# Performance work log

Hardware: AMD Instinct MI355X
Metric: run time of the kernel (lower is better)

The kernel has to match this reference:

```python
import jax, jax.numpy as jnp
import numpy as np

H = 5          # N_LSTM_nodes
NK = 32        # N_kernels
ND = 128       # N_dense_nodes
GH, GW = 20, 22


def _lstm_dir(x, Wih, Whh, b, reverse):
    # x: (P, in_dim); PyTorch gate order i, f, g, o; unbatched sequence of length P
    pre = x @ Wih.T + b  # (P, 4H) input contribution precomputed
    def step(carry, pt):
        h, c = carry
        g = pt + h @ Whh.T
        i, f, gg, o = jnp.split(g, 4)
        c = jax.nn.sigmoid(f) * c + jax.nn.sigmoid(i) * jnp.tanh(gg)
        h = jax.nn.sigmoid(o) * jnp.tanh(c)
        return (h, c), h
    z = jnp.zeros((H,), x.dtype)
    _, hs = jax.lax.scan(step, (z, z), pre, reverse=reverse)
    return hs  # (P, H), aligned with input order


def _bilstm(x, Wih, Whh, b):
    return jnp.concatenate([_lstm_dir(x, Wih[0], Whh[0], b[0], False),
                            _lstm_dir(x, Wih[1], Whh[1], b[1], True)], axis=-1)


def _conv(x, w, b, pad):
    y = jax.lax.conv_general_dilated(x, w, (1, 1), pad,
                                     dimension_numbers=('NCHW', 'OIHW', 'NCHW'))
    return y + b[None, :, None, None]


def _dense(x, w, b):
    return x @ w.T + b


def reference(Traces, Pstart, l0_Wih, l0_Whh, l0_b, l12_Wih, l12_Whh, l12_b,
              cw0, cb0, cw1, cb1, cw2, cb2, cw3, cb3,
              D1_w, D1_b, D2_w, D2_b, D3_w, D3_b,
              X1_w, X1_b, X2_w, X2_b, X3_w, X3_b,
              E1_w, E1_b, E2_w, E2_b, E3_w, E3_b,
              Xs, Ys, EventIndices, NEvents):
    lrelu, relu = jax.nn.leaky_relu, jax.nn.relu
    # 3-layer bidirectional LSTM over the concatenated pixel sequence
    x = _bilstm(Traces, l0_Wih, l0_Whh, l0_b)
    for l in range(2):
        x = _bilstm(x, l12_Wih[l], l12_Whh[l], l12_b[l])
    feat = x[:, 0]                                  # (P,)  LSTM_out[:, 0]
    P = feat.shape[0]
    # scatter: channels 0..H-1 get the LSTM feature, channel H gets Pstart
    vals = jnp.concatenate([jnp.broadcast_to(feat[:, None], (P, H)),
                            Pstart[:, None]], axis=1)          # (P, H+1)
    ch = jnp.arange(H + 1)
    Main = jnp.zeros((NEvents, H + 1, GH, GW), Traces.dtype)
    Main = Main.at[EventIndices[:, None], ch[None, :],
                   Xs[:, None], Ys[:, None]].set(vals)
    Main = jnp.where(jnp.isnan(Main), jnp.asarray(-1.0, Main.dtype), Main)
    Main = lrelu(_conv(Main, cw0, cb0, [(1, 1), (0, 0)]))  # (N, NK, 20, 20)
    Main = lrelu(_conv(Main, cw1, cb1, [(1, 1), (1, 1)]))
    Main = lrelu(_conv(Main, cw2, cb2, [(1, 1), (1, 1)]))
    Main = lrelu(_conv(Main, cw3, cb3, [(1, 1), (1, 1)]))
    Main = Main.reshape(NEvents, -1)                        # (N, NK*20*20)
    Main = relu(_dense(Main, D1_w, D1_b))
    Main = relu(_dense(Main, D2_w, D2_b))
    Main = relu(_dense(Main, D3_w, D3_b))
    Xm = relu(_dense(Main, X1_w, X1_b))
    Xm = relu(_dense(Xm, X2_w, X2_b))
    Xm = _dense(Xm, X3_w, X3_b)
    En = relu(_dense(Main, E1_w, E1_b))
    En = relu(_dense(En, E2_w, E2_b))
    En = _dense(En, E3_w, E3_b)
    out_w = jnp.ones((2,), Main.dtype)  # OutWeights = [1, 1]
    return jnp.concatenate([Xm, En], axis=1) * out_w


def setup_inputs() -> dict:
    key = jax.random.key(0)
    ks = jax.random.split(key, 40)
    P, N = 65536, 4096
    g = lambda i, shape, sc=0.1: jax.random.normal(ks[i], shape, jnp.float32) * sc
    return dict(
        Traces=jax.random.normal(ks[0], (P, 40), jnp.float32),
        Pstart=jax.random.uniform(ks[1], (P,), jnp.float32),
        l0_Wih=g(2, (2, 4 * H, 40)), l0_Whh=g(3, (2, 4 * H, H)), l0_b=g(4, (2, 4 * H)),
        l12_Wih=g(5, (2, 2, 4 * H, 2 * H)), l12_Whh=g(6, (2, 2, 4 * H, H)), l12_b=g(7, (2, 2, 4 * H)),
        cw0=g(8, (NK, H + 1, 3, 3)), cb0=g(9, (NK,)),
        cw1=g(10, (NK, NK, 3, 3)), cb1=g(11, (NK,)),
        cw2=g(12, (NK, NK, 3, 3)), cb2=g(13, (NK,)),
        cw3=g(14, (NK, NK, 3, 3)), cb3=g(15, (NK,)),
        D1_w=g(16, (ND, NK * 20 * 20), 0.01), D1_b=g(17, (ND,)),
        D2_w=g(18, (ND, ND)), D2_b=g(19, (ND,)),
        D3_w=g(20, (ND, ND)), D3_b=g(21, (ND,)),
        X1_w=g(22, (ND, ND)), X1_b=g(23, (ND,)),
        X2_w=g(24, (ND // 2, ND)), X2_b=g(25, (ND // 2,)),
        X3_w=g(26, (1, ND // 2)), X3_b=g(27, (1,)),
        E1_w=g(28, (ND, ND)), E1_b=g(29, (ND,)),
        E2_w=g(30, (ND // 2, ND)), E2_b=g(31, (ND // 2,)),
        E3_w=g(32, (1, ND // 2)), E3_b=g(33, (1,)),
        Xs=jax.random.randint(ks[34], (P,), 0, GH, jnp.int32),
        Ys=jax.random.randint(ks[35], (P,), 0, GW, jnp.int32),
        EventIndices=jnp.sort(jax.random.randint(ks[36], (P,), 0, N, jnp.int32)),
        NEvents=N,
    )
```

## Files before the change

kernel.cpp:

```cpp
#include <hip/hip_runtime.h>
#include <hip/hip_fp16.h>
#include <cstdint>
#include <cstddef>

#define PN 65536
#define NEV 4096
#define LCHUNK 4
#define LHALO 40
#define NCHUNK (PN / LCHUNK)
#define PRS 24

typedef _Float16 half8 __attribute__((ext_vector_type(8)));
typedef _Float16 half4 __attribute__((ext_vector_type(4)));
typedef float    f32x4 __attribute__((ext_vector_type(4)));
typedef float    f32x16 __attribute__((ext_vector_type(16)));

__device__ __forceinline__ float rcpf(float x)  { return __builtin_amdgcn_rcpf(x); }
__device__ __forceinline__ float sigf(float x)  { return rcpf(1.0f + __expf(-x)); }
__device__ __forceinline__ float tanh_(float x) { return 1.0f - 2.0f * rcpf(1.0f + __expf(2.0f * x)); }
__device__ __forceinline__ float lrelu(float x) { return x > 0.0f ? x : 0.01f * x; }

__global__ void k_preL(const float* __restrict__ hin, const float* __restrict__ wih,
                       const float* __restrict__ bb, _Float16* __restrict__ pre, int total) {
  int tid = blockIdx.x * 256 + threadIdx.x;
  if (tid >= total) return;
  int j = tid % 20;
  int p = (tid / 20) % PN;
  int d = tid / (20 * PN);
  const float2* h2 = (const float2*)(hin + (size_t)p * 10);
  const float2* w2 = (const float2*)(wih + (size_t)(d * 20 + j) * 10);
  float acc = bb[d * 20 + j];
  #pragma unroll
  for (int k = 0; k < 5; ++k) {
    float2 a = h2[k], b = w2[k];
    acc = fmaf(a.x, b.x, fmaf(a.y, b.y, acc));
  }
  pre[((size_t)d * PN + p) * PRS + j] = (_Float16)acc;
}

__global__ __launch_bounds__(64, 1) void k_scan(
    const _Float16* __restrict__ pre, const float* __restrict__ whh,
    float* __restrict__ hout, int hstride, int ncomp, int ndir) {
  int tid = blockIdx.x * 64 + threadIdx.x;
  if (tid >= ndir * NCHUNK) return;
  int d = tid / NCHUNK, c = tid % NCHUNK;
  float W[20][5];
  {
    const float4* wd4 = (const float4*)(whh + d * 100);
    float4 wv[25];
    #pragma unroll
    for (int i = 0; i < 25; ++i) wv[i] = wd4[i];
    float* wf = (float*)wv;
    #pragma unroll
    for (int j = 0; j < 20; ++j)
      #pragma unroll
      for (int k = 0; k < 5; ++k) W[j][k] = wf[j * 5 + k];
  }
  const _Float16* pd = pre + (size_t)d * PN * PRS;
  float h[5] = {0, 0, 0, 0, 0}, cs[5] = {0, 0, 0, 0, 0};
  int base = c * LCHUNK;
  int p, step, nsteps;
  if (d == 0) {
    int ps = base - LHALO; if (ps < 0) ps = 0;
    p = ps; step = 1; nsteps = base + LCHUNK - ps;
  } else {
    int ps = base + LCHUNK - 1 + LHALO; if (ps > PN - 1) ps = PN - 1;
    p = ps; step = -1; nsteps = ps - base + 1;
  }

  auto ld = [&](int pp, half8& A, half8& B, half4& C) {
    int pl = pp; if (pl < 0) pl = 0; if (pl >= PN) pl = PN - 1;
    const _Float16* rp = pd + (size_t)pl * PRS;
    A = *(const half8*)rp; B = *(const half8*)(rp + 8); C = *(const half4*)(rp + 16);
  };

  auto STEP = [&](half8 ca, half8 cb, half4 cc) {
    float g[20];
    #pragma unroll
    for (int i = 0; i < 8; ++i) { g[i] = (float)ca[i]; g[8 + i] = (float)cb[i]; }
    #pragma unroll
    for (int i = 0; i < 4; ++i) g[16 + i] = (float)cc[i];
    #pragma unroll
    for (int j = 0; j < 20; ++j) {
      #pragma unroll
      for (int k = 0; k < 5; ++k) g[j] = fmaf(W[j][k], h[k], g[j]);
    }
    #pragma unroll
    for (int k = 0; k < 5; ++k) {
      float it = sigf(g[k]);
      float ft = sigf(g[5 + k]);
      float gt = tanh_(g[10 + k]);
      float ot = sigf(g[15 + k]);
      cs[k] = fmaf(ft, cs[k], it * gt);
      h[k]  = ot * tanh_(cs[k]);
    }
    if ((unsigned)(p - base) < (unsigned)LCHUNK) {
      if (ncomp == 1) {
        hout[p] = h[0];
      } else {
        float* hp = hout + (size_t)p * hstride + d * 5;
        #pragma unroll
        for (int k = 0; k < 5; ++k) hp[k] = h[k];
      }
    }
    p += step;
  };

  half8 a0, a1, a2, a3, b0, b1, b2, b3;
  half4 c0, c1, c2, c3;
  ld(p,            a0, b0, c0);
  ld(p + step,     a1, b1, c1);
  ld(p + 2 * step, a2, b2, c2);
  ld(p + 3 * step, a3, b3, c3);

  for (int s = 0; s < nsteps; s += 4) {
    half8 na0, na1, na2, na3, nb0, nb1, nb2, nb3;
    half4 nc0, nc1, nc2, nc3;
    ld(p + 4 * step, na0, nb0, nc0);
    ld(p + 5 * step, na1, nb1, nc1);
    ld(p + 6 * step, na2, nb2, nc2);
    ld(p + 7 * step, na3, nb3, nc3);
    STEP(a0, b0, c0);
    STEP(a1, b1, c1);
    STEP(a2, b2, c2);
    STEP(a3, b3, c3);
    a0 = na0; b0 = nb0; c0 = nc0;
    a1 = na1; b1 = nb1; c1 = nc1;
    a2 = na2; b2 = nb2; c2 = nc2;
    a3 = na3; b3 = nb3; c3 = nc3;
  }
}

__global__ void k_scat2(const int* __restrict__ ei, const int* __restrict__ xs,
                        const int* __restrict__ ys, const int* __restrict__ owner,
                        const float* __restrict__ feat, const float* __restrict__ pstart,
                        _Float16* __restrict__ main0g) {
  int p = blockIdx.x * 256 + threadIdx.x;
  if (p >= PN) return;
  int e = ei[p];
  int cell = e * 440 + xs[p] * 22 + ys[p];
  if (owner[cell] != p) return;
  _Float16 f = (_Float16)feat[p];
  _Float16* b = main0g + (size_t)cell * 8;
  #pragma unroll
  for (int ch = 0; ch < 5; ++ch) b[ch] = f;
  b[5] = (_Float16)pstart[p];
}

#define PREP_F ((2 * PN * 20) / 256)
#define PREP_A ((NEV * 440 * 4) / 256)
#define PREP_G (PN / 256)
#define PREP_C 144
#define PREP_D (128 * 13)
#define PREP_E 320
__global__ __launch_bounds__(256) void k_prep(
    const float* __restrict__ tr, const float* __restrict__ l0_Wih,
    const float* __restrict__ l0_b, _Float16* __restrict__ pre,
    _Float16* __restrict__ main0g, int* __restrict__ owner,
    const int* __restrict__ ei, const int* __restrict__ xs, const int* __restrict__ ys,
    const float* __restrict__ cw0, const float* __restrict__ cw1,
    const float* __restrict__ cw2, const float* __restrict__ cw3,
    _Float16* __restrict__ wt,
    const float* __restrict__ D1w, _Float16* __restrict__ d1wt,
    const float* __restrict__ D2, const float* __restrict__ D3,
    const float* __restrict__ X1, const float* __restrict__ X2,
    const float* __restrict__ E1, const float* __restrict__ E2,
    _Float16* __restrict__ mlpw) {
  __shared__ float t[32][33];
  int b = blockIdx.x;
  if (b < PREP_F) {
    int tid = b * 256 + threadIdx.x;
    int j = tid % 20;
    int p = (tid / 20) % PN;
    int d = tid / (20 * PN);
    const float4* t4 = (const float4*)(tr + (size_t)p * 40);
    const float4* w4 = (const float4*)(l0_Wih + (size_t)(d * 20 + j) * 40);
    float acc = l0_b[d * 20 + j];
    #pragma unroll
    for (int k = 0; k < 10; ++k) {
      float4 a = t4[k], w = w4[k];
      acc = fmaf(a.x, w.x, fmaf(a.y, w.y, fmaf(a.z, w.z, fmaf(a.w, w.w, acc))));
    }
    pre[((size_t)d * PN + p) * PRS + j] = (_Float16)acc;
  } else if (b < PREP_F + PREP_A) {
    int i = (b - PREP_F) * 256 + threadIdx.x;
    ((uint32_t*)main0g)[i] = 0u;
  } else if (b < PREP_F + PREP_A + PREP_G) {
    int p = (b - PREP_F - PREP_A) * 256 + threadIdx.x;
    int cell = ei[p] * 440 + xs[p] * 22 + ys[p];
    atomicMax(&owner[cell], p);
  } else if (b < PREP_F + PREP_A + PREP_G + PREP_C) {
    int tid = (b - PREP_F - PREP_A - PREP_G) * 256 + threadIdx.x;
    if (tid < 4 * 9216) {
      int L = tid / 9216, r = tid % 9216;
      int ic = r & 31, oc = (r >> 5) & 31, kykx = r >> 10;
      const float* w = (L == 0) ? cw0 : (L == 1) ? cw1 : (L == 2) ? cw2 : cw3;
      int Cin = (L == 0) ? 6 : 32;
      float v = (ic < Cin) ? w[(oc * Cin + ic) * 9 + kykx] : 0.0f;
      wt[tid] = (_Float16)v;
    }
  } else if (b < PREP_F + PREP_A + PREP_G + PREP_C + PREP_D) {
    int j = b - PREP_F - PREP_A - PREP_G - PREP_C;
    int od = j / 13;
    int p0 = (j % 13) * 32;
    int tx = threadIdx.x & 31, ty = threadIdx.x >> 5;
    for (int oc = ty; oc < 32; oc += 8) {
      int pix = p0 + tx;
      t[oc][tx] = (pix < 400) ? D1w[(size_t)od * 12800 + oc * 400 + pix] : 0.0f;
    }
    __syncthreads();
    for (int pp = ty; pp < 32; pp += 8) {
      int pix = p0 + pp;
      if (pix < 400) d1wt[(size_t)od * 12800 + pix * 32 + tx] = (_Float16)t[tx][pp];
    }
  } else {
    int i = (b - PREP_F - PREP_A - PREP_G - PREP_C - PREP_D) * 256 + threadIdx.x;
    if (i < 81920) {
      const float* s; int off;
      if      (i < 16384) { s = D2; off = 0; }
      else if (i < 32768) { s = D3; off = 16384; }
      else if (i < 49152) { s = X1; off = 32768; }
      else if (i < 57344) { s = X2; off = 49152; }
      else if (i < 73728) { s = E1; off = 57344; }
      else                { s = E2; off = 73728; }
      mlpw[i] = (_Float16)s[i - off];
    }
  }
}

#define ARS 28
#define ACT_N (22 * ARS * 40)
__global__ __launch_bounds__(256, 2) void k_conv(
    const _Float16* __restrict__ main0g, const _Float16* __restrict__ wtall,
    const float* __restrict__ cb0, const float* __restrict__ cb1,
    const float* __restrict__ cb2, const float* __restrict__ cb3,
    _Float16* __restrict__ gbuf) {
  __shared__ _Float16 lds[ACT_N];
  int e   = blockIdx.x;
  int tid = threadIdx.x;
  int lane = tid & 63, wv = tid >> 6;
  int ln = lane & 31, s = lane >> 5;

  const uint4* src = (const uint4*)(main0g + (size_t)e * 440 * 8);
  uint4 sv0, sv1;
  int si0 = tid, si1 = tid + 256;
  if (si0 < 440) sv0 = src[si0];
  if (si1 < 440) sv1 = src[si1];

  for (int i = tid; i < 176; i += 256) {
    int row = (i >= 88) ? 21 : 0;
    int j = (i >= 88) ? i - 88 : i;
    int col = j >> 2, hb = (j & 3) * 8;
    *(uint4*)&lds[(row * ARS + col) * 40 + hb] = (uint4){0, 0, 0, 0};
  }
  for (int i = tid; i < 1320; i += 256) {
    int row = 1 + i / 66;
    int j = i % 66;
    int col = j / 3, hb = 8 + (j % 3) * 8;
    *(uint4*)&lds[(row * ARS + col) * 40 + hb] = (uint4){0, 0, 0, 0};
  }
  if (si0 < 440) {
    int r = si0 / 22, c = si0 - r * 22;
    *(uint4*)&lds[((r + 1) * ARS + c) * 40] = sv0;
  }
  if (si1 < 440) {
    int r = si1 / 22, c = si1 - r * 22;
    *(uint4*)&lds[((r + 1) * ARS + c) * 40] = sv1;
  }
  int pix[4]; bool val[4];
  #pragma unroll
  for (int t = 0; t < 4; ++t) {
    int tile = (t < 3) ? (wv + t * 4) : 12;
    int n = tile * 32 + ln;
    val[t] = (n < 400);
    if (n > 399) n = 399;
    int y = n / 20, x = n - y * 20;
    pix[t] = y * ARS + x;
  }
  __syncthreads();

  const float* cbs[4] = {cb0, cb1, cb2, cb3};
  #pragma unroll
  for (int L = 0; L < 4; ++L) {
    const float* cb = cbs[L];
    f32x16 acc[4];
    {
      f32x16 binit;
      #pragma unroll
      for (int g = 0; g < 4; ++g) {
        f32x4 bv = *(const f32x4*)&cb[g * 8 + s * 4];
        #pragma unroll
        for (int j = 0; j < 4; ++j) binit[g * 4 + j] = bv[j];
      }
      #pragma unroll
      for (int t = 0; t < 4; ++t) acc[t] = binit;
    }
    const _Float16* wL = wtall + (size_t)L * 9216;
    #pragma unroll
    for (int h = 0; h < 2; ++h) {
      half8 afr[9];
      #pragma unroll
      for (int tap = 0; tap < 9; ++tap)
        afr[tap] = *(const half8*)&wL[(tap * 32 + ln) * 32 + h * 16 + s * 8];
      #pragma unroll
      for (int t = 0; t < 3; ++t) {
        int base = pix[t] * 40 + h * 16 + s * 8;
        #pragma unroll
        for (int ky = 0; ky < 3; ++ky)
          #pragma unroll
          for (int kx = 0; kx < 3; ++kx) {
            half8 bfr = *(const half8*)&lds[base + (ky * ARS + kx) * 40];
            acc[t] = __builtin_amdgcn_mfma_f32_32x32x16_f16(afr[ky * 3 + kx], bfr, acc[t], 0, 0, 0);
          }
      }
      if (wv == 0) {
        int base = pix[3] * 40 + h * 16 + s * 8;
        #pragma unroll
        for (int ky = 0; ky < 3; ++ky)
          #pragma unroll
          for (int kx = 0; kx < 3; ++kx) {
            half8 bfr = *(const half8*)&lds[base + (ky * ARS + kx) * 40];
            acc[3] = __builtin_amdgcn_mfma_f32_32x32x16_f16(afr[ky * 3 + kx], bfr, acc[3], 0, 0, 0);
          }
      }
      __builtin_amdgcn_sched_barrier(0);
    }
    __syncthreads();
    if (L < 3) {
      #pragma unroll
      for (int t = 0; t < 3; ++t) {
        int wa = (pix[t] + ARS + 1) * 40 + s * 4;
        #pragma unroll
        for (int g = 0; g < 4; ++g) {
          half4 hv;
          #pragma unroll
          for (int j = 0; j < 4; ++j) hv[j] = (_Float16)lrelu(acc[t][g * 4 + j]);
          *(half4*)&lds[wa + g * 8] = hv;
        }
      }
      if (wv == 0 && val[3]) {
        int wa = (pix[3] + ARS + 1) * 40 + s * 4;
        #pragma unroll
        for (int g = 0; g < 4; ++g) {
          half4 hv;
          #pragma unroll
          for (int j = 0; j < 4; ++j) hv[j] = (_Float16)lrelu(acc[3][g * 4 + j]);
          *(half4*)&lds[wa + g * 8] = hv;
        }
      }
      if (L == 0) {
        for (int i = tid; i < 176; i += 256) {
          int r = i >> 3, j = i & 7;
          int c = (j < 4) ? 0 : 21;
          int hb = (j & 3) * 8;
          *(uint4*)&lds[(r * ARS + c) * 40 + hb] = (uint4){0, 0, 0, 0};
        }
      }
      __syncthreads();
    } else {
      #pragma unroll
      for (int t = 0; t < 3; ++t) {
        int n = (wv + t * 4) * 32 + ln;
        _Float16* gp = &gbuf[((size_t)e * 400 + n) * 32 + s * 4];
        #pragma unroll
        for (int g = 0; g < 4; ++g) {
          half4 hv;
          #pragma unroll
          for (int j = 0; j < 4; ++j) hv[j] = (_Float16)lrelu(acc[t][g * 4 + j]);
          *(half4*)&gp[g * 8] = hv;
        }
      }
      if (wv == 0 && val[3]) {
        int n = 384 + ln;
        _Float16* gp = &gbuf[((size_t)e * 400 + n) * 32 + s * 4];
        #pragma unroll
        for (int g = 0; g < 4; ++g) {
          half4 hv;
          #pragma unroll
          for (int j = 0; j < 4; ++j) hv[j] = (_Float16)lrelu(acc[3][g * 4 + j]);
          *(half4*)&gp[g * 8] = hv;
        }
      }
    }
  }
}

__global__ __launch_bounds__(256, 2) void k_d1gemm(const _Float16* __restrict__ A,
    const _Float16* __restrict__ W, float* __restrict__ part) {
  __shared__ _Float16 ldsA[128 * 40];
  __shared__ _Float16 ldsW[128 * 40];
  int e0 = blockIdx.x * 128;
  int k0 = blockIdx.y * 800;
  int tid = threadIdx.x, lane = tid & 63, w = tid >> 6;
  int m_ = lane & 15, q = lane >> 4;
  f32x4 acc[8][2];
  #pragma unroll
  for (int ot = 0; ot < 8; ++ot)
    #pragma unroll
    for (int et = 0; et < 2; ++et) acc[ot][et] = (f32x4){0.f, 0.f, 0.f, 0.f};

  for (int kk = 0; kk < 800; kk += 32) {
    for (int i = tid; i < 512; i += 256) {
      int r = i >> 2, s = i & 3;
      *(uint4*)&ldsA[r * 40 + s * 8] = *(const uint4*)&A[(size_t)(e0 + r) * 12800 + k0 + kk + s * 8];
    }
    for (int i = tid; i < 512; i += 256) {
      int r = i >> 2, s = i & 3;
      *(uint4*)&ldsW[r * 40 + s * 8] = *(const uint4*)&W[(size_t)r * 12800 + k0 + kk + s * 8];
    }
    __syncthreads();
    half8 bfr[2];
    #pragma unroll
    for (int et = 0; et < 2; ++et)
      bfr[et] = *(const half8*)&ldsA[((w * 2 + et) * 16 + m_) * 40 + q * 8];
    #pragma unroll
    for (int ot = 0; ot < 8; ++ot) {
      half8 afr = *(const half8*)&ldsW[(ot * 16 + m_) * 40 + q * 8];
      acc[ot][0] = __builtin_amdgcn_mfma_f32_16x16x32_f16(afr, bfr[0], acc[ot][0], 0, 0, 0);
      acc[ot][1] = __builtin_amdgcn_mfma_f32_16x16x32_f16(afr, bfr[1], acc[ot][1], 0, 0, 0);
    }
    __syncthreads();
  }
  #pragma unroll
  for (int ot = 0; ot < 8; ++ot)
    #pragma unroll
    for (int et = 0; et < 2; ++et) {
      int od = ot * 16 + q * 4;
      int ev = e0 + (w * 2 + et) * 16 + m_;
      *(f32x4*)&part[((size_t)blockIdx.y * NEV + ev) * 128 + od] = acc[ot][et];
    }
}

__global__ __launch_bounds__(256) void k_mlp(
    const float* __restrict__ part, const float* __restrict__ D1_b,
    const _Float16* __restrict__ mlpw,
    const float* __restrict__ D2_b, const float* __restrict__ D3_b,
    const float* __restrict__ X1_b, const float* __restrict__ X2_b,
    const float* __restrict__ X3_w, const float* __restrict__ X3_b,
    const float* __restrict__ E1_b, const float* __restrict__ E2_b,
    const float* __restrict__ E3_w, const float* __restrict__ E3_b,
    float* __restrict__ out) {
  __shared__ _Float16 ldsA[16 * 132];
  __shared__ _Float16 ldsB[16 * 132];
  __shared__ _Float16 ldsW[128 * 132];
  int e0 = blockIdx.x * 16;
  int tid = threadIdx.x, lane = tid & 63, w = tid >> 6;
  int m_ = lane & 15, q = lane >> 4;

  for (int i = tid; i < 2048; i += 256) {
    int ev = i >> 7, od = i & 127;
    float s = D1_b[od];
    #pragma unroll
    for (int sp = 0; sp < 16; ++sp)
      s += part[((size_t)sp * NEV + e0 + ev) * 128 + od];
    ldsA[ev * 132 + od] = (_Float16)fmaxf(s, 0.f);
  }

  auto layer = [&](const _Float16* In, _Float16* Out, int odc,
                   const _Float16* wsrc, const float* bias) {
    const uint4* ws = (const uint4*)wsrc;
    for (int i = tid; i < odc * 16; i += 256) {
      int row = i >> 4, seg = i & 15;
      *(uint4*)&ldsW[row * 132 + seg * 8] = ws[i];
    }
    __syncthreads();
    int tpw = odc >> 6;
    int ot0 = w * tpw;
    half8 bfr[4];
    #pragma unroll
    for (int ks = 0; ks < 4; ++ks)
      bfr[ks] = *(const half8*)&In[m_ * 132 + ks * 32 + q * 8];
    f32x4 acc[2];
    for (int ot = 0; ot < tpw; ++ot) {
      acc[ot] = *(const f32x4*)&bias[(ot0 + ot) * 16 + q * 4];
      #pragma unroll
      for (int ks = 0; ks < 4; ++ks) {
        half8 afr = *(const half8*)&ldsW[((ot0 + ot) * 16 + m_) * 132 + ks * 32 + q * 8];
        acc[ot] = __builtin_amdgcn_mfma_f32_16x16x32_f16(afr, bfr[ks], acc[ot], 0, 0, 0);
      }
    }
    __syncthreads();
    for (int ot = 0; ot < tpw; ++ot) {
      half4 hv;
      #pragma unroll
      for (int r = 0; r < 4; ++r) hv[r] = (_Float16)fmaxf(acc[ot][r], 0.f);
      *(half4*)&Out[m_ * 132 + (ot0 + ot) * 16 + q * 4] = hv;
    }
  };

  __syncthreads();
  layer(ldsA, ldsB, 128, mlpw,          D2_b);
  layer(ldsB, ldsA, 128, mlpw + 16384,  D3_b);
  layer(ldsA, ldsB, 128, mlpw + 32768,  X1_b);
  layer(ldsB, ldsB,  64, mlpw + 49152,  X2_b);
  __syncthreads();
  if (tid < 16) {
    float a = X3_b[0];
    for (int k = 0; k < 64; ++k) a = fmaf((float)ldsB[tid * 132 + k], X3_w[k], a);
    out[(size_t)(e0 + tid) * 2] = a;
  }
  layer(ldsA, ldsB, 128, mlpw + 57344,  E1_b);
  layer(ldsB, ldsB,  64, mlpw + 73728,  E2_b);
  __syncthreads();
  if (tid < 16) {
    float a = E3_b[0];
    for (int k = 0; k < 64; ++k) a = fmaf((float)ldsB[tid * 132 + k], E3_w[k], a);
    out[(size_t)(e0 + tid) * 2 + 1] = a;
  }
}

extern "C" void kernel_launch(void* const* d_in, const int* in_sizes, int n_in,
                              void* d_out, int out_size, void* d_ws, size_t ws_size,
                              hipStream_t stream) {
  const float* Traces  = (const float*)d_in[0];
  const float* Pstart  = (const float*)d_in[1];
  const float* l0_Wih  = (const float*)d_in[2];
  const float* l0_Whh  = (const float*)d_in[3];
  const float* l0_b    = (const float*)d_in[4];
  const float* l12_Wih = (const float*)d_in[5];
  const float* l12_Whh = (const float*)d_in[6];
  const float* l12_b   = (const float*)d_in[7];
  const float* cw0 = (const float*)d_in[8];   const float* cb0 = (const float*)d_in[9];
  const float* cw1 = (const float*)d_in[10];  const float* cb1 = (const float*)d_in[11];
  const float* cw2 = (const float*)d_in[12];  const float* cb2 = (const float*)d_in[13];
  const float* cw3 = (const float*)d_in[14];  const float* cb3 = (const float*)d_in[15];
  const float* D1_w = (const float*)d_in[16]; const float* D1_b = (const float*)d_in[17];
  const float* D2_w = (const float*)d_in[18]; const float* D2_b = (const float*)d_in[19];
  const float* D3_w = (const float*)d_in[20]; const float* D3_b = (const float*)d_in[21];
  const float* X1_w = (const float*)d_in[22]; const float* X1_b = (const float*)d_in[23];
  const float* X2_w = (const float*)d_in[24]; const float* X2_b = (const float*)d_in[25];
  const float* X3_w = (const float*)d_in[26]; const float* X3_b = (const float*)d_in[27];
  const float* E1_w = (const float*)d_in[28]; const float* E1_b = (const float*)d_in[29];
  const float* E2_w = (const float*)d_in[30]; const float* E2_b = (const float*)d_in[31];
  const float* E3_w = (const float*)d_in[32]; const float* E3_b = (const float*)d_in[33];
  const int* Xs = (const int*)d_in[34];
  const int* Ys = (const int*)d_in[35];
  const int* EI = (const int*)d_in[36];
  float* out = (float*)d_out;

  char* wp = (char*)d_ws;
  auto alloc = [&](size_t bytes) -> char* {
    char* p = wp; wp += (bytes + 255) & ~(size_t)255; return p;
  };
  _Float16*  pre    = (_Float16*)alloc(sizeof(_Float16) * 2 * (size_t)PN * PRS);
  float*     hbuf   = (float*)alloc(sizeof(float) * PN * 10);
  float*     feat   = (float*)alloc(sizeof(float) * PN);
  int*       owner  = (int*)alloc(sizeof(int) * NEV * 440);
  _Float16*  main0g = (_Float16*)alloc(sizeof(_Float16) * (size_t)NEV * 440 * 8);
  _Float16*  gbuf   = (_Float16*)alloc(sizeof(_Float16) * (size_t)NEV * 12800);
  _Float16*  wtall  = (_Float16*)alloc(sizeof(_Float16) * 4 * 9216);
  _Float16*  d1wt   = (_Float16*)alloc(sizeof(_Float16) * 128 * 12800);
  _Float16*  mlpw   = (_Float16*)alloc(sizeof(_Float16) * 81920);
  float*     d1part = (float*)owner;

  k_prep<<<PREP_F + PREP_A + PREP_G + PREP_C + PREP_D + PREP_E, 256, 0, stream>>>(
      Traces, l0_Wih, l0_b, pre,
      main0g, owner, EI, Xs, Ys,
      cw0, cw1, cw2, cw3, wtall, D1_w, d1wt,
      D2_w, D3_w, X1_w, X2_w, E1_w, E2_w, mlpw);

  k_scan<<<(2 * NCHUNK) / 64, 64, 0, stream>>>(pre, l0_Whh, hbuf, 10, 5, 2);
  k_preL<<<(2 * PN * 20) / 256, 256, 0, stream>>>(hbuf, l12_Wih, l12_b, pre, 2 * PN * 20);
  k_scan<<<(2 * NCHUNK) / 64, 64, 0, stream>>>(pre, l12_Whh, hbuf, 10, 5, 2);
  k_preL<<<(PN * 20) / 256, 256, 0, stream>>>(hbuf, l12_Wih + 400, l12_b + 40, pre, PN * 20);
  k_scan<<<NCHUNK / 64, 64, 0, stream>>>(pre, l12_Whh + 200, feat, 1, 1, 1);

  k_scat2<<<PN / 256, 256, 0, stream>>>(EI, Xs, Ys, owner, feat, Pstart, main0g);

  k_conv<<<NEV, 256, 0, stream>>>(main0g, wtall, cb0, cb1, cb2, cb3, gbuf);

  dim3 g1(32, 16);
  k_d1gemm<<<g1, 256, 0, stream>>>(gbuf, d1wt, d1part);
  k_mlp<<<NEV / 16, 256, 0, stream>>>(d1part, D1_b, mlpw, D2_b, D3_b, X1_b, X2_b, X3_w, X3_b,
                                      E1_b, E2_b, E3_w, E3_b, out);
}
```

Before: 477.8 us.

## Fuse next-layer input projection into LSTM scan epilogue with per-direction partial sums

The separate input-projection kernels and the intermediate hidden-state buffer are removed. Each scan thread now stages its chunk's hidden states in shared memory, then computes its direction's partial contribution to the next layer's gate pre-activations and writes them as fp32. The next scan adds the forward and backward partials when it loads each step. This removes two launches and the hidden-state round trip through memory. In exchange, each step now reads wider fp32 rows instead of packed fp16, and the prefetch depth drops from four steps ahead to one.

```diff
diff --git a/kernel.cpp b/kernel.cpp
--- a/kernel.cpp
+++ b/kernel.cpp
@@ -20,30 +20,14 @@
 __device__ __forceinline__ float tanh_(float x) { return 1.0f - 2.0f * rcpf(1.0f + __expf(2.0f * x)); }
 __device__ __forceinline__ float lrelu(float x) { return x > 0.0f ? x : 0.01f * x; }
 
-__global__ void k_preL(const float* __restrict__ hin, const float* __restrict__ wih,
-                       const float* __restrict__ bb, _Float16* __restrict__ pre, int total) {
-  int tid = blockIdx.x * 256 + threadIdx.x;
-  if (tid >= total) return;
-  int j = tid % 20;
-  int p = (tid / 20) % PN;
-  int d = tid / (20 * PN);
-  const float2* h2 = (const float2*)(hin + (size_t)p * 10);
-  const float2* w2 = (const float2*)(wih + (size_t)(d * 20 + j) * 10);
-  float acc = bb[d * 20 + j];
-  #pragma unroll
-  for (int k = 0; k < 5; ++k) {
-    float2 a = h2[k], b = w2[k];
-    acc = fmaf(a.x, b.x, fmaf(a.y, b.y, acc));
-  }
-  pre[((size_t)d * PN + p) * PRS + j] = (_Float16)acc;
-}
-
-__global__ __launch_bounds__(64, 1) void k_scan(
+
+__global__ __launch_bounds__(64, 1) void k_scanA(
     const _Float16* __restrict__ pre, const float* __restrict__ whh,
-    float* __restrict__ hout, int hstride, int ncomp, int ndir) {
+    const float* __restrict__ wihn, const float* __restrict__ bn,
+    float* __restrict__ po) {
+  __shared__ float hsv[64][4][5];
   int tid = blockIdx.x * 64 + threadIdx.x;
-  if (tid >= ndir * NCHUNK) return;
-  int d = tid / NCHUNK, c = tid % NCHUNK;
+  int d = tid / NCHUNK, c = tid - d * NCHUNK;
   float W[20][5];
   {
     const float4* wd4 = (const float4*)(whh + d * 100);
@@ -94,14 +78,10 @@
       cs[k] = fmaf(ft, cs[k], it * gt);
       h[k]  = ot * tanh_(cs[k]);
     }
-    if ((unsigned)(p - base) < (unsigned)LCHUNK) {
-      if (ncomp == 1) {
-        hout[p] = h[0];
-      } else {
-        float* hp = hout + (size_t)p * hstride + d * 5;
-        #pragma unroll
-        for (int k = 0; k < 5; ++k) hp[k] = h[k];
-      }
+    unsigned u = (unsigned)(p - base);
+    if (u < (unsigned)LCHUNK) {
+      #pragma unroll
+      for (int k = 0; k < 5; ++k) hsv[threadIdx.x][u][k] = h[k];
     }
     p += step;
   };
@@ -128,6 +108,144 @@
     a1 = na1; b1 = nb1; c1 = nc1;
     a2 = na2; b2 = nb2; c2 = nc2;
     a3 = na3; b3 = nb3; c3 = nc3;
+  }
+
+  float Wp[40][5];
+  #pragma unroll
+  for (int j = 0; j < 40; ++j) {
+    int addr = ((j >= 20) ? (200 + (j - 20) * 10) : (j * 10)) + d * 5;
+    #pragma unroll
+    for (int k = 0; k < 5; ++k) Wp[j][k] = wihn[addr + k];
+  }
+  #pragma unroll
+  for (int oi = 0; oi < 4; ++oi) {
+    float hv[5];
+    #pragma unroll
+    for (int k = 0; k < 5; ++k) hv[k] = hsv[threadIdx.x][oi][k];
+    float pr[40];
+    #pragma unroll
+    for (int j = 0; j < 40; ++j) {
+      float a = (d == 0) ? bn[j] : 0.0f;
+      #pragma unroll
+      for (int k = 0; k < 5; ++k) a = fmaf(Wp[j][k], hv[k], a);
+      pr[j] = a;
+    }
+    float* dst = po + (size_t)(base + oi) * 80 + d * 40;
+    #pragma unroll
+    for (int q = 0; q < 10; ++q) {
+      float4 v; v.x = pr[q * 4]; v.y = pr[q * 4 + 1]; v.z = pr[q * 4 + 2]; v.w = pr[q * 4 + 3];
+      *(float4*)&dst[q * 4] = v;
+    }
+  }
+}
+
+__global__ __launch_bounds__(64, 1) void k_scanB(
+    const float* __restrict__ pre32, const float* __restrict__ whh,
+    const float* __restrict__ wihn, const float* __restrict__ bn,
+    float* __restrict__ po, float* __restrict__ feat, int ndir, int rstride) {
+  __shared__ float hsv[64][4][5];
+  int tid = blockIdx.x * 64 + threadIdx.x;
+  if (tid >= ndir * NCHUNK) return;
+  int d = tid / NCHUNK, c = tid - d * NCHUNK;
+  int soff = rstride >> 1;
+  float W[20][5];
+  {
+    const float4* wd4 = (const float4*)(whh + d * 100);
+    float4 wv[25];
+    #pragma unroll
+    for (int i = 0; i < 25; ++i) wv[i] = wd4[i];
+    float* wf = (float*)wv;
+    #pragma unroll
+    for (int j = 0; j < 20; ++j)
+      #pragma unroll
+      for (int k = 0; k < 5; ++k) W[j][k] = wf[j * 5 + k];
+  }
+  float h[5] = {0, 0, 0, 0, 0}, cs[5] = {0, 0, 0, 0, 0};
+  int base = c * LCHUNK;
+  int p, step, nsteps;
+  if (d == 0) {
+    int ps = base - LHALO; if (ps < 0) ps = 0;
+    p = ps; step = 1; nsteps = base + LCHUNK - ps;
+  } else {
+    int ps = base + LCHUNK - 1 + LHALO; if (ps > PN - 1) ps = PN - 1;
+    p = ps; step = -1; nsteps = ps - base + 1;
+  }
+
+  auto ld32 = [&](int pp, f32x4* S) {
+    int pl = pp; if (pl < 0) pl = 0; if (pl >= PN) pl = PN - 1;
+    const float* r0 = pre32 + (size_t)pl * rstride + d * 20;
+    const float* r1 = r0 + soff;
+    #pragma unroll
+    for (int q = 0; q < 5; ++q) S[q] = *(const f32x4*)&r0[q * 4];
+    #pragma unroll
+    for (int q = 0; q < 5; ++q) S[5 + q] = *(const f32x4*)&r1[q * 4];
+  };
+
+  auto STEP = [&](const f32x4* S) {
+    float g[20];
+    #pragma unroll
+    for (int j = 0; j < 20; ++j) g[j] = S[j >> 2][j & 3] + S[5 + (j >> 2)][j & 3];
+    #pragma unroll
+    for (int j = 0; j < 20; ++j) {
+      #pragma unroll
+      for (int k = 0; k < 5; ++k) g[j] = fmaf(W[j][k], h[k], g[j]);
+    }
+    #pragma unroll
+    for (int k = 0; k < 5; ++k) {
+      float it = sigf(g[k]);
+      float ft = sigf(g[5 + k]);
+      float gt = tanh_(g[10 + k]);
+      float ot = sigf(g[15 + k]);
+      cs[k] = fmaf(ft, cs[k], it * gt);
+      h[k]  = ot * tanh_(cs[k]);
+    }
+    unsigned u = (unsigned)(p - base);
+    if (u < (unsigned)LCHUNK) {
+      if (feat) {
+        feat[p] = h[0];
+      } else {
+        #pragma unroll
+        for (int k = 0; k < 5; ++k) hsv[threadIdx.x][u][k] = h[k];
+      }
+    }
+    p += step;
+  };
+
+  f32x4 S0[10], S1[10];
+  ld32(p, S0);
+  for (int s = 0; s < nsteps; s += 2) {
+    ld32(p + step, S1);
+    STEP(S0);
+    ld32(p + step, S0);
+    STEP(S1);
+  }
+
+  if (!feat) {
+    float Wp[20][5];
+    #pragma unroll
+    for (int j = 0; j < 20; ++j)
+      #pragma unroll
+      for (int k = 0; k < 5; ++k) Wp[j][k] = wihn[j * 10 + d * 5 + k];
+    #pragma unroll
+    for (int oi = 0; oi < 4; ++oi) {
+      float hv[5];
+      #pragma unroll
+      for (int k = 0; k < 5; ++k) hv[k] = hsv[threadIdx.x][oi][k];
+      float pr[20];
+      #pragma unroll
+      for (int j = 0; j < 20; ++j) {
+        float a = (d == 0) ? bn[j] : 0.0f;
+        #pragma unroll
+        for (int k = 0; k < 5; ++k) a = fmaf(Wp[j][k], hv[k], a);
+        pr[j] = a;
+      }
+      float* dst = po + (size_t)(base + oi) * 40 + d * 20;
+      #pragma unroll
+      for (int q = 0; q < 5; ++q) {
+        float4 v; v.x = pr[q * 4]; v.y = pr[q * 4 + 1]; v.z = pr[q * 4 + 2]; v.w = pr[q * 4 + 3];
+        *(float4*)&dst[q * 4] = v;
+      }
+    }
   }
 }
 
@@ -543,7 +661,6 @@
     char* p = wp; wp += (bytes + 255) & ~(size_t)255; return p;
   };
   _Float16*  pre    = (_Float16*)alloc(sizeof(_Float16) * 2 * (size_t)PN * PRS);
-  float*     hbuf   = (float*)alloc(sizeof(float) * PN * 10);
   float*     feat   = (float*)alloc(sizeof(float) * PN);
   int*       owner  = (int*)alloc(sizeof(int) * NEV * 440);
   _Float16*  main0g = (_Float16*)alloc(sizeof(_Float16) * (size_t)NEV * 440 * 8);
@@ -552,6 +669,8 @@
   _Float16*  d1wt   = (_Float16*)alloc(sizeof(_Float16) * 128 * 12800);
   _Float16*  mlpw   = (_Float16*)alloc(sizeof(_Float16) * 81920);
   float*     d1part = (float*)owner;
+  float*     pre1   = (float*)gbuf;
+  float*     pre2   = (float*)gbuf + (size_t)PN * 80;
 
   k_prep<<<PREP_F + PREP_A + PREP_G + PREP_C + PREP_D + PREP_E, 256, 0, stream>>>(
       Traces, l0_Wih, l0_b, pre,
@@ -559,11 +678,11 @@
       cw0, cw1, cw2, cw3, wtall, D1_w, d1wt,
       D2_w, D3_w, X1_w, X2_w, E1_w, E2_w, mlpw);
 
-  k_scan<<<(2 * NCHUNK) / 64, 64, 0, stream>>>(pre, l0_Whh, hbuf, 10, 5, 2);
-  k_preL<<<(2 * PN * 20) / 256, 256, 0, stream>>>(hbuf, l12_Wih, l12_b, pre, 2 * PN * 20);
-  k_scan<<<(2 * NCHUNK) / 64, 64, 0, stream>>>(pre, l12_Whh, hbuf, 10, 5, 2);
-  k_preL<<<(PN * 20) / 256, 256, 0, stream>>>(hbuf, l12_Wih + 400, l12_b + 40, pre, PN * 20);
-  k_scan<<<NCHUNK / 64, 64, 0, stream>>>(pre, l12_Whh + 200, feat, 1, 1, 1);
+  k_scanA<<<(2 * NCHUNK) / 64, 64, 0, stream>>>(pre, l0_Whh, l12_Wih, l12_b, pre1);
+  k_scanB<<<(2 * NCHUNK) / 64, 64, 0, stream>>>(pre1, l12_Whh, l12_Wih + 400, l12_b + 40,
+                                                pre2, nullptr, 2, 80);
+  k_scanB<<<NCHUNK / 64, 64, 0, stream>>>(pre2, l12_Whh + 200, nullptr, nullptr,
+                                          nullptr, feat, 1, 40);
 
   k_scat2<<<PN / 256, 256, 0, stream>>>(EI, Xs, Ys, owner, feat, Pstart, main0g);
 
```

After: 475.2 us (median of 2 runs). No clear change (-0.5%).
